# Performance work log

Hardware: AMD Instinct MI355X
Metric: run time of the kernel (lower is better)

The kernel has to match this reference:

```python
import jax, jax.numpy as jnp
import numpy as np

N_NODES = 40000
N_EDGES = 640000
IN, HID, OUT = 128, 128, 47


def setup_inputs() -> dict:
    key = jax.random.key(0)
    ks = jax.random.split(key, 12)
    def glorot(k, shape):
        fan = sum(shape)
        return jax.random.normal(k, shape, dtype=jnp.float32) * jnp.sqrt(2.0 / fan)
    return {
        "x": jax.random.normal(ks[0], (N_NODES, IN), dtype=jnp.float32),
        "src": jax.random.randint(ks[1], (N_EDGES,), 0, N_NODES),
        "dst": jax.random.randint(ks[2], (N_EDGES,), 0, N_NODES),
        "W_self0": glorot(ks[3], (IN, HID)),
        "W_neigh0": glorot(ks[4], (IN, HID)),
        "b0": jnp.zeros((HID,), dtype=jnp.float32),
        "W_self1": glorot(ks[5], (HID, HID)),
        "W_neigh1": glorot(ks[6], (HID, HID)),
        "b1": jnp.zeros((HID,), dtype=jnp.float32),
        "W_self2": glorot(ks[7], (HID, OUT)),
        "W_neigh2": glorot(ks[8], (HID, OUT)),
        "b2": jnp.zeros((OUT,), dtype=jnp.float32),
    }


def _sage_conv(h, src, dst, W_self, W_neigh, b):
    # DGL SAGEConv('mean'): mean of neighbor (src) feats scattered to dst,
    # then fc_neigh(h_neigh) + fc_self(h_self) + bias.
    n = h.shape[0]
    deg = jax.ops.segment_sum(jnp.ones_like(dst, dtype=h.dtype), dst, num_segments=n)
    agg = jax.ops.segment_sum(h[src], dst, num_segments=n)          # [N, d] gather + scatter-add
    h_neigh = agg / jnp.maximum(deg, 1.0)[:, None]                   # isolated nodes -> 0 (DGL behavior)
    return h @ W_self + h_neigh @ W_neigh + b


def reference(x, src, dst, W_self0, W_neigh0, b0, W_self1, W_neigh1, b1,
              W_self2, W_neigh2, b2):
    # Dropout is identity in eval mode; omitted here.
    h = _sage_conv(x, src, dst, W_self0, W_neigh0, b0)
    h = jax.nn.relu(h)
    h = _sage_conv(h, src, dst, W_self1, W_neigh1, b1)
    h = jax.nn.relu(h)
    h = _sage_conv(h, src, dst, W_self2, W_neigh2, b2)
    return h
```

## Files before the change

kernel.cpp:

```cpp
#include <hip/hip_runtime.h>
#include <hip/hip_bf16.h>
#include <stdint.h>

#define NN 40000
#define NE 640000
#define NB 157

typedef __attribute__((ext_vector_type(8))) short bf16x8;
typedef __attribute__((ext_vector_type(4))) float f32x4;
typedef __attribute__((ext_vector_type(2))) float f32x2v;

static __device__ __forceinline__ unsigned short f2b(float f) {
    unsigned b = __float_as_uint(f);
    return (unsigned short)((b + 0x7FFFu + ((b >> 16) & 1u)) >> 16);
}
static __device__ __forceinline__ float blo(unsigned v) { return __uint_as_float(v << 16); }
static __device__ __forceinline__ float bhi(unsigned v) { return __uint_as_float(v & 0xffff0000u); }

static __device__ __forceinline__ void acc4(float* a, uint2 v) {
    a[0] += blo(v.x); a[1] += bhi(v.x);
    a[2] += blo(v.y); a[3] += bhi(v.y);
}


#if __has_builtin(__builtin_amdgcn_cvt_pk_fp8_f32) && __has_builtin(__builtin_amdgcn_cvt_pk_f32_fp8)
#define FP8_HW 1
#else
#define FP8_HW 0
#endif

static __device__ __forceinline__ unsigned char f2fp8_sw(float f) {
    f = fminf(fmaxf(f, -448.f), 448.f);
    unsigned b = __float_as_uint(f);
    unsigned s = (b >> 24) & 0x80u;
    unsigned ab = b & 0x7fffffffu;
    if (ab < 0x3c000000u) return (unsigned char)s;
    unsigned r = ab + 0x7ffffu + ((ab >> 20) & 1u);
    unsigned e = ((r >> 23) - 120u) & 0xfu;
    unsigned m = (r >> 20) & 7u;
    return (unsigned char)(s | (e << 3) | m);
}
static __device__ __forceinline__ float fp82f_sw(unsigned char u) {
    unsigned s = ((unsigned)u & 0x80u) << 24;
    unsigned e = (u >> 3) & 15u, m = u & 7u;
    float nrm = __uint_as_float(s | ((e + 120u) << 23) | (m << 20));
    float dnm = __uint_as_float(s | 0x3f800000u) * (float)m * 0.001953125f;
    return e ? nrm : dnm;
}

static __device__ __forceinline__ unsigned pack_fp8x4(float a, float b, float c, float d) {
#if FP8_HW
    int v = __builtin_amdgcn_cvt_pk_fp8_f32(a, b, 0, false);
    v = __builtin_amdgcn_cvt_pk_fp8_f32(c, d, v, true);
    return (unsigned)v;
#else
    return (unsigned)f2fp8_sw(a) | ((unsigned)f2fp8_sw(b) << 8) |
           ((unsigned)f2fp8_sw(c) << 16) | ((unsigned)f2fp8_sw(d) << 24);
#endif
}

static __device__ __forceinline__ void acc4f8(float* a, unsigned v) {
#if FP8_HW
    f32x2v p0 = __builtin_amdgcn_cvt_pk_f32_fp8((int)v, false);
    f32x2v p1 = __builtin_amdgcn_cvt_pk_f32_fp8((int)v, true);
    a[0] += p0.x; a[1] += p0.y; a[2] += p1.x; a[3] += p1.y;
#else
    a[0] += fp82f_sw(v & 0xff);         a[1] += fp82f_sw((v >> 8) & 0xff);
    a[2] += fp82f_sw((v >> 16) & 0xff); a[3] += fp82f_sw(v >> 24);
#endif
}
static __device__ __forceinline__ void acc16f8(float* a, uint4 v) {
    acc4f8(a, v.x); acc4f8(a + 4, v.y); acc4f8(a + 8, v.z); acc4f8(a + 12, v.w);
}


__global__ void count_deg_kernel(const int* __restrict__ dst, int* __restrict__ deg, int n) {
    int i = blockIdx.x * blockDim.x + threadIdx.x;
    if (i < n) atomicAdd(&deg[dst[i]], 1);
}

__global__ __launch_bounds__(256) void scan1_kernel(const int* __restrict__ deg,
                                                    int* __restrict__ bsum) {
    int i = blockIdx.x * 256 + threadIdx.x;
    int v = (i < NN) ? deg[i] : 0;
#pragma unroll
    for (int off = 1; off < 64; off <<= 1) v += __shfl_xor(v, off);
    __shared__ int ws4[4];
    if ((threadIdx.x & 63) == 0) ws4[threadIdx.x >> 6] = v;
    __syncthreads();
    if (threadIdx.x == 0) bsum[blockIdx.x] = ws4[0] + ws4[1] + ws4[2] + ws4[3];
}

__global__ void scan_top_kernel(const int* __restrict__ bsum, int* __restrict__ btop) {
    int lane = threadIdx.x;
    int run = 0;
    for (int base = 0; base < NB; base += 64) {
        int idx = base + lane;
        int v = (idx < NB) ? bsum[idx] : 0;
        int s = v;
#pragma unroll
        for (int off = 1; off < 64; off <<= 1) { int t = __shfl_up(s, off); if (lane >= off) s += t; }
        if (idx < NB) btop[idx] = run + s - v;
        run += __shfl(s, 63);
    }
}

__global__ __launch_bounds__(256) void scan2_kernel(const int* __restrict__ deg,
                                                    const int* __restrict__ btop,
                                                    int* __restrict__ row_ptr) {
    int b = blockIdx.x;
    int i = b * 256 + threadIdx.x;
    int lane = threadIdx.x & 63, wv = threadIdx.x >> 6;
    int v = (i < NN) ? deg[i] : 0;
    int s = v;
#pragma unroll
    for (int off = 1; off < 64; off <<= 1) { int t = __shfl_up(s, off); if (lane >= off) s += t; }
    __shared__ int wsum[4];
    if (lane == 63) wsum[wv] = s;
    __syncthreads();
    int add = btop[b];
    for (int w = 0; w < wv; ++w) add += wsum[w];
    if (i < NN) row_ptr[i] = add + s - v;
    if (i == NN - 1) row_ptr[NN] = add + s;
}

__global__ void fill_csr_kernel(const int* __restrict__ src, const int* __restrict__ dst,
                                const int* __restrict__ row_ptr, int* __restrict__ cursor,
                                int* __restrict__ csr, int n) {
    int i = blockIdx.x * blockDim.x + threadIdx.x;
    if (i < n) {
        int d = dst[i];
        int pos = row_ptr[d] + atomicAdd(&cursor[d], 1);
        csr[pos] = src[i];
    }
}


__global__ __launch_bounds__(256) void prep_kernel(
    const float* __restrict__ x,
    const float* __restrict__ Ws0, const float* __restrict__ Wn0,
    const float* __restrict__ Ws1, const float* __restrict__ Wn1,
    const float* __restrict__ Ws2, const float* __restrict__ Wn2,
    int* __restrict__ zero_base, unsigned short* __restrict__ X,
    unsigned char* __restrict__ X8, unsigned char* __restrict__ H18,
    unsigned short* __restrict__ Wt0, unsigned short* __restrict__ Wt1,
    unsigned short* __restrict__ Wt2s, unsigned short* __restrict__ Wt2n) {
    int b = blockIdx.x, tid = threadIdx.x;
    if (b < 79) {
        int i = (b * 256 + tid) * 4;
        if (i < 80000) *(int4*)(zero_base + i) = (int4){0, 0, 0, 0};
    } else if (b < 5079) {
        int i = (b - 79) * 256 + tid;
        int e = i << 2;
        float4 v = *(const float4*)(x + e);
        uint2 o;
        o.x = f2b(v.x) | ((unsigned)f2b(v.y) << 16);
        o.y = f2b(v.z) | ((unsigned)f2b(v.w) << 16);
        *(uint2*)(X + e) = o;
        *(unsigned*)(X8 + e) = pack_fp8x4(v.x, v.y, v.z, v.w);
    } else if (b < 5383) {
        int i = (b - 5079) * 256 + tid;
        if (i < 65536) {
            int l = i >> 15, j = i & 32767;
            int n = j >> 8, k = j & 255;
            const float* Ws = l ? Ws1 : Ws0;
            const float* Wn = l ? Wn1 : Wn0;
            float v = (k < 128) ? Ws[k * 128 + n] : Wn[(k - 128) * 128 + n];
            (l ? Wt1 : Wt0)[n * 256 + k] = f2b(v);
        } else if (i < 65536 + 6144) {
            int j = i - 65536;
            int n = j >> 7, k = j & 127;
            float v = (n < 47) ? Ws2[k * 47 + n] : 0.f;
            Wt2s[n * 128 + k] = f2b(v);
        } else if (i < 65536 + 12288) {
            int j = i - 65536 - 6144;
            int n = j >> 7, k = j & 127;
            float v = (n < 47) ? Wn2[k * 47 + n] : 0.f;
            Wt2n[n * 128 + k] = f2b(v);
        }
    } else {
        if (tid < 16) *(uint2*)(X8 + (size_t)NN * 128 + tid * 8) = (uint2){0, 0};
        else if (tid < 32) *(uint2*)(H18 + (size_t)NN * 128 + (tid - 16) * 8) = (uint2){0, 0};
    }
}


template <bool RELU, bool WFP8>
__global__ __launch_bounds__(256) void sage_layer_kernel(
    const unsigned short* __restrict__ Hin, const unsigned char* __restrict__ H8in,
    const int* __restrict__ csr, const int* __restrict__ row_ptr,
    const unsigned short* __restrict__ Wt, const float* __restrict__ bias,
    unsigned short* __restrict__ Hout, unsigned char* __restrict__ H8out) {
    __shared__ unsigned short agg_lds[16 * 128];

    int tid = threadIdx.x;
    int wv = tid >> 6, lane = tid & 63;
    int lr = lane & 15, lg = lane >> 4;
    int lr8 = lane & 7, g = lane >> 3;
    int t = g >> 1, sub = g & 1;
    int m0 = blockIdx.x * 16;

    int nb = m0 + wv * 4;
    int rp5 = (lane < 5) ? row_ptr[nb + lane] : 0;
    int beg = __shfl(rp5, t), end = __shfl(rp5, t + 1);
    int deg = end - beg;
    int half = (deg + 1) >> 1;
    int js = beg + sub * half;
    int je = sub ? end : beg + half;
    int last = (je > js) ? je - 1 : js;

    float a[16] = {};
    for (int j = js; j < je; j += 4) {
        int j1 = j + 1, j2 = j + 2, j3 = j + 3;
        int iA = csr[j];
        int iBr = csr[min(j1, last)];
        int iCr = csr[min(j2, last)];
        int iDr = csr[min(j3, last)];
        int iB = (j1 < je) ? iBr : NN;
        int iC = (j2 < je) ? iCr : NN;
        int iD = (j3 < je) ? iDr : NN;
        uint4 vA = *(const uint4*)(H8in + (size_t)iA * 128 + lr8 * 16);
        uint4 vB = *(const uint4*)(H8in + (size_t)iB * 128 + lr8 * 16);
        uint4 vC = *(const uint4*)(H8in + (size_t)iC * 128 + lr8 * 16);
        uint4 vD = *(const uint4*)(H8in + (size_t)iD * 128 + lr8 * 16);
        acc16f8(a, vA); acc16f8(a, vB); acc16f8(a, vC); acc16f8(a, vD);
    }
#pragma unroll
    for (int k = 0; k < 16; ++k) a[k] += __shfl_xor(a[k], 8);

    if (sub == 0) {
        float inv = 1.0f / fmaxf((float)deg, 1.0f);
        uint4 o0, o1;
        o0.x = f2b(a[0] * inv)  | ((unsigned)f2b(a[1] * inv) << 16);
        o0.y = f2b(a[2] * inv)  | ((unsigned)f2b(a[3] * inv) << 16);
        o0.z = f2b(a[4] * inv)  | ((unsigned)f2b(a[5] * inv) << 16);
        o0.w = f2b(a[6] * inv)  | ((unsigned)f2b(a[7] * inv) << 16);
        o1.x = f2b(a[8] * inv)  | ((unsigned)f2b(a[9] * inv) << 16);
        o1.y = f2b(a[10] * inv) | ((unsigned)f2b(a[11] * inv) << 16);
        o1.z = f2b(a[12] * inv) | ((unsigned)f2b(a[13] * inv) << 16);
        o1.w = f2b(a[14] * inv) | ((unsigned)f2b(a[15] * inv) << 16);
        int row = wv * 4 + t;
        *(uint4*)&agg_lds[row * 128 + ((2 * lr8) ^ row) * 8] = o0;
        *(uint4*)&agg_lds[row * 128 + ((2 * lr8 + 1) ^ row) * 8] = o1;
    }
    __syncthreads();

    bf16x8 afr[8];
#pragma unroll
    for (int kt = 0; kt < 4; ++kt)
        afr[kt] = *(const bf16x8*)(Hin + (size_t)(m0 + lr) * 128 + kt * 32 + lg * 8);
#pragma unroll
    for (int kt = 0; kt < 4; ++kt) {
        int chunk = (kt * 4 + lg) ^ lr;
        afr[4 + kt] = *(const bf16x8*)&agg_lds[lr * 128 + chunk * 8];
    }

    int n0 = (wv * 2) * 16 + lr;
    int n1 = n0 + 16;
    f32x4 acc0 = (f32x4){0.f, 0.f, 0.f, 0.f};
    f32x4 acc1 = (f32x4){0.f, 0.f, 0.f, 0.f};
#pragma unroll
    for (int kt = 0; kt < 8; ++kt) {
        bf16x8 b0 = *(const bf16x8*)(Wt + (size_t)n0 * 256 + kt * 32 + lg * 8);
        bf16x8 b1 = *(const bf16x8*)(Wt + (size_t)n1 * 256 + kt * 32 + lg * 8);
        acc0 = __builtin_amdgcn_mfma_f32_16x16x32_bf16(afr[kt], b0, acc0, 0, 0, 0);
        acc1 = __builtin_amdgcn_mfma_f32_16x16x32_bf16(afr[kt], b1, acc1, 0, 0, 0);
    }

    float bs0 = bias[n0], bs1 = bias[n1];
#pragma unroll
    for (int r = 0; r < 4; ++r) {
        int m = m0 + lg * 4 + r;
        float v0 = acc0[r] + bs0;
        float v1 = acc1[r] + bs1;
        if (RELU) { v0 = fmaxf(v0, 0.f); v1 = fmaxf(v1, 0.f); }
        Hout[(size_t)m * 128 + n0] = f2b(v0);
        Hout[(size_t)m * 128 + n1] = f2b(v1);
        if (WFP8) {
#if FP8_HW
            H8out[(size_t)m * 128 + n0] =
                (unsigned char)(__builtin_amdgcn_cvt_pk_fp8_f32(v0, v0, 0, false) & 0xff);
            H8out[(size_t)m * 128 + n1] =
                (unsigned char)(__builtin_amdgcn_cvt_pk_fp8_f32(v1, v1, 0, false) & 0xff);
#else
            H8out[(size_t)m * 128 + n0] = f2fp8_sw(v0);
            H8out[(size_t)m * 128 + n1] = f2fp8_sw(v1);
#endif
        }
    }
}


__global__ __launch_bounds__(192) void dual_gemm_kernel(
    const unsigned short* __restrict__ H2,
    const unsigned short* __restrict__ Wt2s, const unsigned short* __restrict__ Wt2n,
    const float* __restrict__ b2,
    float* __restrict__ out, unsigned short* __restrict__ Hn) {
    int wv = threadIdx.x >> 6, lane = threadIdx.x & 63;
    int lr = lane & 15, lg = lane >> 4;

    bf16x8 bfr[2][4];
    float bs[2];
#pragma unroll
    for (int c = 0; c < 2; ++c) {
        int t = wv * 2 + c;
        bool is_s = t < 3;
        int n = (is_s ? t : t - 3) * 16 + lr;
        const unsigned short* W = is_s ? Wt2s : Wt2n;
#pragma unroll
        for (int kt = 0; kt < 4; ++kt)
            bfr[c][kt] = *(const bf16x8*)(W + (size_t)n * 128 + kt * 32 + lg * 8);
        bs[c] = (is_s && n < 47) ? b2[n] : 0.f;
    }

    for (int tt = 0; tt < 2; ++tt) {
        int m0 = blockIdx.x * 32 + tt * 16;
        bf16x8 afr[4];
#pragma unroll
        for (int kt = 0; kt < 4; ++kt)
            afr[kt] = *(const bf16x8*)(H2 + (size_t)(m0 + lr) * 128 + kt * 32 + lg * 8);
        f32x4 acc[2];
#pragma unroll
        for (int c = 0; c < 2; ++c) acc[c] = (f32x4){0.f, 0.f, 0.f, 0.f};
#pragma unroll
        for (int kt = 0; kt < 4; ++kt)
#pragma unroll
            for (int c = 0; c < 2; ++c)
                acc[c] = __builtin_amdgcn_mfma_f32_16x16x32_bf16(afr[kt], bfr[c][kt], acc[c], 0, 0, 0);
#pragma unroll
        for (int c = 0; c < 2; ++c) {
            int t = wv * 2 + c;
            bool is_s = t < 3;
            int n = (is_s ? t : t - 3) * 16 + lr;
#pragma unroll
            for (int r = 0; r < 4; ++r) {
                int m = m0 + lg * 4 + r;
                float v = acc[c][r] + bs[c];
                if (is_s) {
                    if (n < 47) out[(size_t)m * 47 + n] = v;
                } else {
                    Hn[(size_t)m * 64 + n] = f2b(v);
                }
            }
        }
    }
}


__global__ void aggregate_out_kernel(const unsigned short* __restrict__ Hn,
                                     const int* __restrict__ csr,
                                     const int* __restrict__ row_ptr,
                                     float* __restrict__ out) {
    int node = (blockIdx.x * blockDim.x + threadIdx.x) >> 6;
    int lane = threadIdx.x & 63;
    if (node >= NN) return;
    int eg = lane >> 4, lc = lane & 15;
    int beg = row_ptr[node], end = row_ptr[node + 1];
    float a[4] = {};
    int j = beg + eg;
    for (; j + 12 < end; j += 16) {
        int s0 = csr[j], s1 = csr[j + 4], s2 = csr[j + 8], s3 = csr[j + 12];
        uint2 v0 = *(const uint2*)(Hn + (size_t)s0 * 64 + lc * 4);
        uint2 v1 = *(const uint2*)(Hn + (size_t)s1 * 64 + lc * 4);
        uint2 v2 = *(const uint2*)(Hn + (size_t)s2 * 64 + lc * 4);
        uint2 v3 = *(const uint2*)(Hn + (size_t)s3 * 64 + lc * 4);
        acc4(a, v0); acc4(a, v1); acc4(a, v2); acc4(a, v3);
    }
    for (; j < end; j += 4) {
        uint2 v = *(const uint2*)(Hn + (size_t)csr[j] * 64 + lc * 4);
        acc4(a, v);
    }
#pragma unroll
    for (int k = 0; k < 4; ++k) {
        a[k] += __shfl_xor(a[k], 16);
        a[k] += __shfl_xor(a[k], 32);
    }
    if (eg == 0 && lc < 12) {
        float inv = 1.0f / fmaxf((float)(end - beg), 1.0f);
        int c0 = lc * 4;
#pragma unroll
        for (int r = 0; r < 4; ++r)
            if (c0 + r < 47) out[(size_t)node * 47 + c0 + r] += a[r] * inv;
    }
}


extern "C" void kernel_launch(void* const* d_in, const int* in_sizes, int n_in,
                              void* d_out, int out_size, void* d_ws, size_t ws_size,
                              hipStream_t stream) {
    const float* x   = (const float*)d_in[0];
    const int*   src = (const int*)d_in[1];
    const int*   dst = (const int*)d_in[2];
    const float* Ws0 = (const float*)d_in[3];
    const float* Wn0 = (const float*)d_in[4];
    const float* b0  = (const float*)d_in[5];
    const float* Ws1 = (const float*)d_in[6];
    const float* Wn1 = (const float*)d_in[7];
    const float* b1  = (const float*)d_in[8];
    const float* Ws2 = (const float*)d_in[9];
    const float* Wn2 = (const float*)d_in[10];
    const float* b2  = (const float*)d_in[11];
    float* out = (float*)d_out;

    uintptr_t p = ((uintptr_t)d_ws + 255) & ~(uintptr_t)255;
    auto take = [&](size_t bytes) {
        void* r = (void*)p;
        p = (p + bytes + 255) & ~(uintptr_t)255;
        return r;
    };
    int* deg     = (int*)take(40000 * 4);
    int* cursor  = (int*)take(40000 * 4);
    int* row_ptr = (int*)take(40004 * 4);
    int* csr     = (int*)take(640000 * 4);
    unsigned short* X   = (unsigned short*)take((size_t)NN * 128 * 2);
    unsigned short* H1  = (unsigned short*)take((size_t)NN * 128 * 2);
    unsigned short* H2  = X;
    unsigned short* Wt0 = (unsigned short*)take(128 * 256 * 2);
    unsigned short* Wt1 = (unsigned short*)take(128 * 256 * 2);
    unsigned short* Wt2s = (unsigned short*)take(48 * 128 * 2);
    unsigned short* Wt2n = (unsigned short*)take(48 * 128 * 2);
    unsigned short* Hn  = (unsigned short*)take((size_t)NN * 64 * 2);
    int* bsum = (int*)take(NB * 4);
    int* btop = (int*)take(NB * 4);
    unsigned char* X8  = (unsigned char*)take((size_t)(NN + 1) * 128);
    unsigned char* H18 = (unsigned char*)take((size_t)(NN + 1) * 128);

    prep_kernel<<<5384, 256, 0, stream>>>(x, Ws0, Wn0, Ws1, Wn1, Ws2, Wn2,
                                          deg, X, X8, H18, Wt0, Wt1, Wt2s, Wt2n);
    count_deg_kernel<<<2500, 256, 0, stream>>>(dst, deg, NE);
    scan1_kernel<<<NB, 256, 0, stream>>>(deg, bsum);
    scan_top_kernel<<<1, 64, 0, stream>>>(bsum, btop);
    scan2_kernel<<<NB, 256, 0, stream>>>(deg, btop, row_ptr);
    fill_csr_kernel<<<2500, 256, 0, stream>>>(src, dst, row_ptr, cursor, csr, NE);

    sage_layer_kernel<true, true><<<2500, 256, 0, stream>>>(X, X8, csr, row_ptr, Wt0, b0, H1, H18);
    sage_layer_kernel<true, false><<<2500, 256, 0, stream>>>(H1, H18, csr, row_ptr, Wt1, b1, H2, nullptr);
    dual_gemm_kernel<<<1250, 192, 0, stream>>>(H2, Wt2s, Wt2n, b2, out, Hn);
    aggregate_out_kernel<<<10000, 256, 0, stream>>>(Hn, csr, row_ptr, out);
}
```

Before: 181.2 us.

## Fuse degree count into prep, widen gather unroll, restructure output aggregation

Degree counting moves into the prep kernel, with a memset zeroing deg and cursor, which removes one kernel launch. The neighbor gather loops in the SAGE layer and the output aggregation now issue eight independent indexed loads per iteration instead of four, exposing more memory-level parallelism. The output aggregation assigns two nodes per wave with split edge halves and padded sentinel rows, replacing the per-node four-way edge split. The self-feature A-fragment loads are hoisted ahead of the gather to overlap their latency, at the cost of more live registers.

```diff
diff --git a/kernel.cpp b/kernel.cpp
--- a/kernel.cpp
+++ b/kernel.cpp
@@ -74,11 +74,6 @@
 }
 
 
-__global__ void count_deg_kernel(const int* __restrict__ dst, int* __restrict__ deg, int n) {
-    int i = blockIdx.x * blockDim.x + threadIdx.x;
-    if (i < n) atomicAdd(&deg[dst[i]], 1);
-}
-
 __global__ __launch_bounds__(256) void scan1_kernel(const int* __restrict__ deg,
                                                     int* __restrict__ bsum) {
     int i = blockIdx.x * 256 + threadIdx.x;
@@ -137,20 +132,21 @@
 
 
 __global__ __launch_bounds__(256) void prep_kernel(
-    const float* __restrict__ x,
+    const float* __restrict__ x, const int* __restrict__ dst,
     const float* __restrict__ Ws0, const float* __restrict__ Wn0,
     const float* __restrict__ Ws1, const float* __restrict__ Wn1,
     const float* __restrict__ Ws2, const float* __restrict__ Wn2,
-    int* __restrict__ zero_base, unsigned short* __restrict__ X,
+    int* __restrict__ deg, unsigned short* __restrict__ X,
     unsigned char* __restrict__ X8, unsigned char* __restrict__ H18,
+    unsigned short* __restrict__ Hn,
     unsigned short* __restrict__ Wt0, unsigned short* __restrict__ Wt1,
     unsigned short* __restrict__ Wt2s, unsigned short* __restrict__ Wt2n) {
     int b = blockIdx.x, tid = threadIdx.x;
-    if (b < 79) {
-        int i = (b * 256 + tid) * 4;
-        if (i < 80000) *(int4*)(zero_base + i) = (int4){0, 0, 0, 0};
-    } else if (b < 5079) {
-        int i = (b - 79) * 256 + tid;
+    if (b < 2500) {
+        int i = b * 256 + tid;
+        atomicAdd(&deg[dst[i]], 1);
+    } else if (b < 7500) {
+        int i = (b - 2500) * 256 + tid;
         int e = i << 2;
         float4 v = *(const float4*)(x + e);
         uint2 o;
@@ -158,8 +154,8 @@
         o.y = f2b(v.z) | ((unsigned)f2b(v.w) << 16);
         *(uint2*)(X + e) = o;
         *(unsigned*)(X8 + e) = pack_fp8x4(v.x, v.y, v.z, v.w);
-    } else if (b < 5383) {
-        int i = (b - 5079) * 256 + tid;
+    } else if (b < 7804) {
+        int i = (b - 7500) * 256 + tid;
         if (i < 65536) {
             int l = i >> 15, j = i & 32767;
             int n = j >> 8, k = j & 255;
@@ -172,7 +168,7 @@
             int n = j >> 7, k = j & 127;
             float v = (n < 47) ? Ws2[k * 47 + n] : 0.f;
             Wt2s[n * 128 + k] = f2b(v);
-        } else if (i < 65536 + 12288) {
+        } else {
             int j = i - 65536 - 6144;
             int n = j >> 7, k = j & 127;
             float v = (n < 47) ? Wn2[k * 47 + n] : 0.f;
@@ -181,6 +177,7 @@
     } else {
         if (tid < 16) *(uint2*)(X8 + (size_t)NN * 128 + tid * 8) = (uint2){0, 0};
         else if (tid < 32) *(uint2*)(H18 + (size_t)NN * 128 + (tid - 16) * 8) = (uint2){0, 0};
+        else if (tid < 48) *(uint2*)((unsigned char*)(Hn + (size_t)NN * 64) + (tid - 32) * 8) = (uint2){0, 0};
     }
 }
 
@@ -199,6 +196,11 @@
     int lr8 = lane & 7, g = lane >> 3;
     int t = g >> 1, sub = g & 1;
     int m0 = blockIdx.x * 16;
+
+    bf16x8 afr[8];
+#pragma unroll
+    for (int kt = 0; kt < 4; ++kt)
+        afr[kt] = *(const bf16x8*)(Hin + (size_t)(m0 + lr) * 128 + kt * 32 + lg * 8);
 
     int nb = m0 + wv * 4;
     int rp5 = (lane < 5) ? row_ptr[nb + lane] : 0;
@@ -210,20 +212,19 @@
     int last = (je > js) ? je - 1 : js;
 
     float a[16] = {};
-    for (int j = js; j < je; j += 4) {
-        int j1 = j + 1, j2 = j + 2, j3 = j + 3;
-        int iA = csr[j];
-        int iBr = csr[min(j1, last)];
-        int iCr = csr[min(j2, last)];
-        int iDr = csr[min(j3, last)];
-        int iB = (j1 < je) ? iBr : NN;
-        int iC = (j2 < je) ? iCr : NN;
-        int iD = (j3 < je) ? iDr : NN;
-        uint4 vA = *(const uint4*)(H8in + (size_t)iA * 128 + lr8 * 16);
-        uint4 vB = *(const uint4*)(H8in + (size_t)iB * 128 + lr8 * 16);
-        uint4 vC = *(const uint4*)(H8in + (size_t)iC * 128 + lr8 * 16);
-        uint4 vD = *(const uint4*)(H8in + (size_t)iD * 128 + lr8 * 16);
-        acc16f8(a, vA); acc16f8(a, vB); acc16f8(a, vC); acc16f8(a, vD);
+    for (int j = js; j < je; j += 8) {
+        int idxs[8];
+#pragma unroll
+        for (int k = 0; k < 8; ++k) idxs[k] = csr[min(j + k, last)];
+#pragma unroll
+        for (int k = 0; k < 8; ++k)
+            if (j + k >= je) idxs[k] = NN;
+        uint4 v[8];
+#pragma unroll
+        for (int k = 0; k < 8; ++k)
+            v[k] = *(const uint4*)(H8in + (size_t)idxs[k] * 128 + lr8 * 16);
+#pragma unroll
+        for (int k = 0; k < 8; ++k) acc16f8(a, v[k]);
     }
 #pragma unroll
     for (int k = 0; k < 16; ++k) a[k] += __shfl_xor(a[k], 8);
@@ -245,10 +246,6 @@
     }
     __syncthreads();
 
-    bf16x8 afr[8];
-#pragma unroll
-    for (int kt = 0; kt < 4; ++kt)
-        afr[kt] = *(const bf16x8*)(Hin + (size_t)(m0 + lr) * 128 + kt * 32 + lg * 8);
 #pragma unroll
     for (int kt = 0; kt < 4; ++kt) {
         int chunk = (kt * 4 + lg) ^ lr;
@@ -347,36 +344,43 @@
 }
 
 
-__global__ void aggregate_out_kernel(const unsigned short* __restrict__ Hn,
-                                     const int* __restrict__ csr,
-                                     const int* __restrict__ row_ptr,
-                                     float* __restrict__ out) {
-    int node = (blockIdx.x * blockDim.x + threadIdx.x) >> 6;
+__global__ __launch_bounds__(256) void aggregate_out_kernel(
+    const unsigned short* __restrict__ Hn, const int* __restrict__ csr,
+    const int* __restrict__ row_ptr, float* __restrict__ out) {
+    int wave = (blockIdx.x * blockDim.x + threadIdx.x) >> 6;
     int lane = threadIdx.x & 63;
-    if (node >= NN) return;
-    int eg = lane >> 4, lc = lane & 15;
-    int beg = row_ptr[node], end = row_ptr[node + 1];
+    int nb = wave * 2;
+    if (nb >= NN) return;
+    int t = lane >> 5, sub = (lane >> 4) & 1, lc = lane & 15;
+    int rp3 = (lane < 3) ? row_ptr[nb + lane] : 0;
+    int beg = __shfl(rp3, t), end = __shfl(rp3, t + 1);
+    int deg = end - beg;
+    int half = (deg + 1) >> 1;
+    int js = beg + sub * half;
+    int je = sub ? end : beg + half;
+    int last = (je > js) ? je - 1 : js;
+
     float a[4] = {};
-    int j = beg + eg;
-    for (; j + 12 < end; j += 16) {
-        int s0 = csr[j], s1 = csr[j + 4], s2 = csr[j + 8], s3 = csr[j + 12];
-        uint2 v0 = *(const uint2*)(Hn + (size_t)s0 * 64 + lc * 4);
-        uint2 v1 = *(const uint2*)(Hn + (size_t)s1 * 64 + lc * 4);
-        uint2 v2 = *(const uint2*)(Hn + (size_t)s2 * 64 + lc * 4);
-        uint2 v3 = *(const uint2*)(Hn + (size_t)s3 * 64 + lc * 4);
-        acc4(a, v0); acc4(a, v1); acc4(a, v2); acc4(a, v3);
-    }
-    for (; j < end; j += 4) {
-        uint2 v = *(const uint2*)(Hn + (size_t)csr[j] * 64 + lc * 4);
-        acc4(a, v);
-    }
-#pragma unroll
-    for (int k = 0; k < 4; ++k) {
-        a[k] += __shfl_xor(a[k], 16);
-        a[k] += __shfl_xor(a[k], 32);
-    }
-    if (eg == 0 && lc < 12) {
-        float inv = 1.0f / fmaxf((float)(end - beg), 1.0f);
+    for (int j = js; j < je; j += 8) {
+        int idxs[8];
+#pragma unroll
+        for (int k = 0; k < 8; ++k) idxs[k] = csr[min(j + k, last)];
+#pragma unroll
+        for (int k = 0; k < 8; ++k)
+            if (j + k >= je) idxs[k] = NN;
+        uint2 v[8];
+#pragma unroll
+        for (int k = 0; k < 8; ++k)
+            v[k] = *(const uint2*)(Hn + (size_t)idxs[k] * 64 + lc * 4);
+#pragma unroll
+        for (int k = 0; k < 8; ++k) acc4(a, v[k]);
+    }
+#pragma unroll
+    for (int k = 0; k < 4; ++k) a[k] += __shfl_xor(a[k], 16);
+
+    if (sub == 0 && lc < 12) {
+        float inv = 1.0f / fmaxf((float)deg, 1.0f);
+        int node = nb + t;
         int c0 = lc * 4;
 #pragma unroll
         for (int r = 0; r < 4; ++r)
@@ -419,15 +423,15 @@
     unsigned short* Wt1 = (unsigned short*)take(128 * 256 * 2);
     unsigned short* Wt2s = (unsigned short*)take(48 * 128 * 2);
     unsigned short* Wt2n = (unsigned short*)take(48 * 128 * 2);
-    unsigned short* Hn  = (unsigned short*)take((size_t)NN * 64 * 2);
+    unsigned short* Hn  = (unsigned short*)take((size_t)(NN + 1) * 64 * 2);
     int* bsum = (int*)take(NB * 4);
     int* btop = (int*)take(NB * 4);
     unsigned char* X8  = (unsigned char*)take((size_t)(NN + 1) * 128);
     unsigned char* H18 = (unsigned char*)take((size_t)(NN + 1) * 128);
 
-    prep_kernel<<<5384, 256, 0, stream>>>(x, Ws0, Wn0, Ws1, Wn1, Ws2, Wn2,
-                                          deg, X, X8, H18, Wt0, Wt1, Wt2s, Wt2n);
-    count_deg_kernel<<<2500, 256, 0, stream>>>(dst, deg, NE);
+    hipMemsetAsync(deg, 0, 80000 * sizeof(int), stream);
+    prep_kernel<<<7805, 256, 0, stream>>>(x, dst, Ws0, Wn0, Ws1, Wn1, Ws2, Wn2,
+                                          deg, X, X8, H18, Hn, Wt0, Wt1, Wt2s, Wt2n);
     scan1_kernel<<<NB, 256, 0, stream>>>(deg, bsum);
     scan_top_kernel<<<1, 64, 0, stream>>>(bsum, btop);
     scan2_kernel<<<NB, 256, 0, stream>>>(deg, btop, row_ptr);
@@ -436,5 +440,5 @@
     sage_layer_kernel<true, true><<<2500, 256, 0, stream>>>(X, X8, csr, row_ptr, Wt0, b0, H1, H18);
     sage_layer_kernel<true, false><<<2500, 256, 0, stream>>>(H1, H18, csr, row_ptr, Wt1, b1, H2, nullptr);
     dual_gemm_kernel<<<1250, 192, 0, stream>>>(H2, Wt2s, Wt2n, b2, out, Hn);
-    aggregate_out_kernel<<<10000, 256, 0, stream>>>(Hn, csr, row_ptr, out);
-}
+    aggregate_out_kernel<<<5000, 256, 0, stream>>>(Hn, csr, row_ptr, out);
+}
```

Measured after the change: 180.1 us. No clear change (-0.6%).
